# Performance work log

Hardware: AMD Instinct MI355X
Metric: run time of the kernel (lower is better)

The kernel has to match this reference:

```python
import jax, jax.numpy as jnp
import numpy as np

B, N, D, L = 16, 100, 1024, 2000


def setup_inputs() -> dict:
    key = jax.random.key(0)
    ks = jax.random.split(key, 9)
    s = 1.0 / np.sqrt(D)
    return {
        "feature": jax.random.normal(ks[0], (B, N, D), dtype=jnp.float32),
        "graph": jax.random.randint(ks[1], (B, N, N), 0, L),
        "W0": jax.random.normal(ks[2], (D, D), dtype=jnp.float32) * s,
        "W1": jax.random.normal(ks[3], (D, D), dtype=jnp.float32) * s,
        "bias": jax.random.uniform(ks[4], (L, D), dtype=jnp.float32, minval=-s, maxval=s),
        "dp_Wa": jax.random.normal(ks[5], (D, D), dtype=jnp.float32) * s,
        "dp_ba": jax.random.normal(ks[6], (D,), dtype=jnp.float32) * s,
        "dp_Wb": jax.random.normal(ks[7], (D, D), dtype=jnp.float32) * s,
        "dp_bb": jax.random.normal(ks[8], (D,), dtype=jnp.float32) * s,
        "get_alpha": 0,
    }


def reference(feature, graph, W0, W1, bias, dp_Wa, dp_ba, dp_Wb, dp_bb, get_alpha):
    # ---- DirectedGraphConv.conv ----
    adj = (graph != 0).astype(feature.dtype)                     # [B,N,N]
    out = feature + feature @ W0.T + feature @ W1.T              # [B,N,D]
    out = out + jnp.take(bias, graph, axis=0).sum(axis=2)        # label-embedding gather+sum over neighbors
    # ---- relation_alpha: DotProduct(feature, feature) ----
    a = feature @ dp_Wa.T + dp_ba                                # [B,N,D]
    b = feature @ dp_Wb.T + dp_bb                                # [B,N,D]
    alpha = jnp.einsum('bik,bjk->bij', a, b)                     # [B,N,N]
    alpha = jnp.maximum(alpha, 0.0)                              # alpha[alpha<0]=0
    alpha = jnp.einsum('bij,bjk->bik', adj, alpha)               # bmm(adj, alpha)
    alpha = jax.nn.softmax(alpha, axis=1)                        # Softmax(dim=1)
    out = jnp.einsum('bij,bjk->bik', alpha, out)                 # bmm(alpha, output)
    if get_alpha:
        return (out, alpha)
    return out
```

## Files before the change

kernel.cpp:

```cpp
#include <hip/hip_runtime.h>
#include <stdint.h>

#define B_   16
#define N_   100
#define D_   1024
#define L_   2000
#define M_   1600

#define ZCAP 64
#define RCAP 24
#define TC   12

typedef __bf16 bf16x8 __attribute__((ext_vector_type(8)));
typedef float  f32x4  __attribute__((ext_vector_type(4)));

__device__ __forceinline__ void gl_lds16(const __bf16* g, __bf16* l) {
    __builtin_amdgcn_global_load_lds(
        (const __attribute__((address_space(1))) void*)g,
        (__attribute__((address_space(3))) void*)l, 16, 0, 0);
}


__global__ void __launch_bounds__(256)
k_prep(const float* __restrict__ f,
       const float* __restrict__ W0, const float* __restrict__ W1,
       const float* __restrict__ Wa, const float* __restrict__ Wb,
       const float* __restrict__ bias,
       __bf16* __restrict__ fb, __bf16* __restrict__ wcat, __bf16* __restrict__ biasB) {
    int i = blockIdx.x * 256 + threadIdx.x;
    union { __bf16 h[8]; uint4 u; } pk;
    if (i < 204800) {
        long base = (long)i * 8;
        const float4* p = (const float4*)(f + base);
        float4 x = p[0], y = p[1];
        pk.h[0]=(__bf16)x.x; pk.h[1]=(__bf16)x.y; pk.h[2]=(__bf16)x.z; pk.h[3]=(__bf16)x.w;
        pk.h[4]=(__bf16)y.x; pk.h[5]=(__bf16)y.y; pk.h[6]=(__bf16)y.z; pk.h[7]=(__bf16)y.w;
        ((uint4*)fb)[i] = pk.u;
    } else if (i < 598016) {
        int j = i - 204800;
        long base = (long)j * 8;
        long seg = base >> 20;
        long off = base & ((1l << 20) - 1);
        if (seg == 0) {
            const float4* p0 = (const float4*)(W0 + off);
            const float4* p1 = (const float4*)(W1 + off);
            float4 a0 = p0[0], a1 = p0[1], b0 = p1[0], b1 = p1[1];
            pk.h[0]=(__bf16)(a0.x+b0.x); pk.h[1]=(__bf16)(a0.y+b0.y);
            pk.h[2]=(__bf16)(a0.z+b0.z); pk.h[3]=(__bf16)(a0.w+b0.w);
            pk.h[4]=(__bf16)(a1.x+b1.x); pk.h[5]=(__bf16)(a1.y+b1.y);
            pk.h[6]=(__bf16)(a1.z+b1.z); pk.h[7]=(__bf16)(a1.w+b1.w);
        } else {
            const float* src = (seg == 1) ? Wa : Wb;
            const float4* p = (const float4*)(src + off);
            float4 x = p[0], y = p[1];
            pk.h[0]=(__bf16)x.x; pk.h[1]=(__bf16)x.y; pk.h[2]=(__bf16)x.z; pk.h[3]=(__bf16)x.w;
            pk.h[4]=(__bf16)y.x; pk.h[5]=(__bf16)y.y; pk.h[6]=(__bf16)y.z; pk.h[7]=(__bf16)y.w;
        }
        ((uint4*)wcat)[j] = pk.u;
    } else {
        int j = i - 598016;
        long base = (long)j * 8;
        const float4* p = (const float4*)(bias + base);
        float4 x = p[0], y = p[1];
        pk.h[0]=(__bf16)x.x; pk.h[1]=(__bf16)x.y; pk.h[2]=(__bf16)x.z; pk.h[3]=(__bf16)x.w;
        pk.h[4]=(__bf16)y.x; pk.h[5]=(__bf16)y.y; pk.h[6]=(__bf16)y.z; pk.h[7]=(__bf16)y.w;
        ((uint4*)biasB)[j] = pk.u;
    }
}


#define BM 64
#define BN 128
#define BK 64

__global__ void __launch_bounds__(256)
k_gemm(const __bf16* __restrict__ A, const __bf16* __restrict__ Bw,
       const float* __restrict__ feat, const float* __restrict__ ba,
       const float* __restrict__ bbias,
       float* __restrict__ out0, float* __restrict__ aB, float* __restrict__ bB) {
    __shared__ __align__(16) __bf16 As[BM * BK];
    __shared__ __align__(16) __bf16 Bs[BN * BK];
    int t = threadIdx.x;
    int bm = blockIdx.x, bn = blockIdx.y;
    int lane = t & 63, wave = t >> 6;
    int wr = wave & 1, wc = wave >> 1;
    int lrow = lane & 15, quad = lane >> 4;

    f32x4 acc[2][4] = {};
    const __bf16* Ag = A  + (long)(bm * BM) * D_;
    const __bf16* Bg = Bw + (long)(bn * BN) * D_;

    for (int k0 = 0; k0 < D_; k0 += BK) {
        #pragma unroll
        for (int pi = 0; pi < 2; ++pi) {
            int p = pi * 256 + t, row = p >> 3, c = (p & 7) ^ (row & 7);
            gl_lds16(Ag + (long)row * D_ + k0 + c * 8, As + p * 8);
        }
        #pragma unroll
        for (int pi = 0; pi < 4; ++pi) {
            int p = pi * 256 + t, row = p >> 3, c = (p & 7) ^ (row & 7);
            gl_lds16(Bg + (long)row * D_ + k0 + c * 8, Bs + p * 8);
        }
        __syncthreads();
        #pragma unroll
        for (int ks = 0; ks < 2; ++ks) {
            bf16x8 af[2], bf[4];
            #pragma unroll
            for (int i = 0; i < 2; ++i) {
                int r = wr * 32 + i * 16 + lrow;
                int slot = r * 8 + (((ks << 2) | quad) ^ (r & 7));
                af[i] = *(const bf16x8*)(As + slot * 8);
            }
            #pragma unroll
            for (int j = 0; j < 4; ++j) {
                int r = wc * 64 + j * 16 + lrow;
                int slot = r * 8 + (((ks << 2) | quad) ^ (r & 7));
                bf[j] = *(const bf16x8*)(Bs + slot * 8);
            }
            #pragma unroll
            for (int i = 0; i < 2; ++i)
                #pragma unroll
                for (int j = 0; j < 4; ++j)
                    acc[i][j] = __builtin_amdgcn_mfma_f32_16x16x32_bf16(af[i], bf[j], acc[i][j], 0, 0, 0);
        }
        __syncthreads();
    }

    int nbase = bn * BN;
    int seg = nbase >> 10;
    #pragma unroll
    for (int i = 0; i < 2; ++i) {
        int gm0 = bm * BM + wr * 32 + i * 16 + quad * 4;
        #pragma unroll
        for (int j = 0; j < 4; ++j) {
            int col = (nbase + wc * 64 + j * 16 + lrow) & 1023;
            #pragma unroll
            for (int r = 0; r < 4; ++r) {
                long m = gm0 + r;
                float v = acc[i][j][r];
                if (seg == 0)      out0[m * D_ + col] = v + feat[m * D_ + col];
                else if (seg == 1) aB[m * D_ + col]   = v + ba[col];
                else               bB[m * D_ + col]   = v + bbias[col];
            }
        }
    }
}


__global__ void __launch_bounds__(256)
k_gather(const int* __restrict__ graph, const __bf16* __restrict__ biasB,
         float* __restrict__ out0) {
    int bi = blockIdx.x;
    int t = threadIdx.x;
    __shared__ int idxs[N_];
    if (t < N_) idxs[t] = graph[(long)bi * N_ + t];
    __syncthreads();
    float a0 = 0.f, a1 = 0.f, a2 = 0.f, a3 = 0.f;
    for (int j = 0; j < N_; ++j) {
        int lb = idxs[j];
        union { uint2 u; __bf16 h[4]; } pk;
        pk.u = ((const uint2*)(biasB + (long)lb * D_))[t];
        a0 += (float)pk.h[0]; a1 += (float)pk.h[1];
        a2 += (float)pk.h[2]; a3 += (float)pk.h[3];
    }
    float4* o = (float4*)(out0 + (long)bi * D_) + t;
    float4 cur = *o;
    cur.x += a0; cur.y += a1; cur.z += a2; cur.w += a3;
    *o = cur;
}


__global__ void __launch_bounds__(256)
k_scan(const int* __restrict__ graph, int* __restrict__ meta) {
    int b = blockIdx.x, t = threadIdx.x;
    __shared__ int cnt, ndvS;
    __shared__ int zi[ZCAP], zj[ZCAP], pr[ZCAP], di[RCAP];
    if (t == 0) cnt = 0;
    __syncthreads();
    const int* g = graph + (long)b * N_ * N_;
    for (int p = t; p < N_ * N_; p += 256) {
        if (g[p] == 0) {
            int pos = atomicAdd(&cnt, 1);
            if (pos < ZCAP) { zi[pos] = p / N_; zj[pos] = p % N_; }
        }
    }
    __syncthreads();
    if (t == 0) {
        int Z = min(cnt, ZCAP), n = 0;
        for (int q = 0; q < Z; ++q) {
            int r = -1;
            for (int s = 0; s < n; ++s) if (di[s] == zi[q]) { r = s; break; }
            if (r < 0 && n < RCAP) { di[n] = zi[q]; r = n; ++n; }
            pr[q] = r;
        }
        ndvS = n;
    }
    __syncthreads();
    int Z = min(cnt, ZCAP), n = ndvS;
    int* mb = meta + b * 256;
    if (t == 0) { mb[0] = Z; mb[1] = n; }
    if (t < Z) { mb[2 + t] = zj[t]; mb[66 + t] = pr[t]; }
    if (t < n) mb[130 + t] = di[t];
    if (t < N_) {
        int m = 0;
        for (int r = 0; r < n; ++r) if (di[r] == t) m = 1 + r;
        mb[154 + t] = m;
    }
}


__global__ void __launch_bounds__(256)
k_alpha(const int* __restrict__ meta, const float* __restrict__ aB,
        const float* __restrict__ bB, float* __restrict__ wl, float* __restrict__ cwG) {
    int b = blockIdx.x, kc = blockIdx.y;
    int t = threadIdx.x, lane = t & 63, wave = t >> 6;
    const int* mb = meta + b * 256;
    int Z = mb[0], ndv = mb[1];
    __shared__ int zjL[ZCAP], prL[ZCAP];
    __shared__ float corrL[RCAP][4];
    __shared__ float wred[4][4];
    if (t < Z) { zjL[t] = mb[2 + t]; prL[t] = mb[66 + t]; }
    if (t < RCAP * 4) corrL[t >> 2][t & 3] = 0.f;
    __syncthreads();

    int k0 = kc * 4;
    float4 bv[4];
    #pragma unroll
    for (int kk = 0; kk < 4; ++kk)
        bv[kk] = *(const float4*)(bB + ((long)(b * N_ + k0 + kk)) * D_ + t * 4);

    for (int q = 0; q < Z; ++q) {
        const float* ar = aB + ((long)(b * N_ + zjL[q])) * D_;
        float4 av = *(const float4*)(ar + t * 4);
        float s[4];
        #pragma unroll
        for (int kk = 0; kk < 4; ++kk)
            s[kk] = av.x * bv[kk].x + av.y * bv[kk].y + av.z * bv[kk].z + av.w * bv[kk].w;
        #pragma unroll
        for (int off = 32; off > 0; off >>= 1)
            #pragma unroll
            for (int kk = 0; kk < 4; ++kk) s[kk] += __shfl_xor(s[kk], off);
        if (lane == 0) { wred[wave][0]=s[0]; wred[wave][1]=s[1]; wred[wave][2]=s[2]; wred[wave][3]=s[3]; }
        __syncthreads();
        if (t < 4) {
            float v = wred[0][t] + wred[1][t] + wred[2][t] + wred[3][t];
            v = fmaxf(v, 0.f);
            int r = prL[q];
            if (r >= 0) corrL[r][t] += v;
        }
        __syncthreads();
    }

    if (t < 4) {
        int k = k0 + t;
        float denom = (float)(N_ - ndv);
        for (int r = 0; r < ndv; ++r) {
            float e = __expf(-corrL[r][t]);
            corrL[r][t] = e;
            denom += e;
        }
        float w = 1.f / denom;
        wl[b * N_ + k] = w;
        for (int r = 0; r < ndv; ++r)
            cwG[((long)b * RCAP + r) * N_ + k] = corrL[r][t] * w;
    }
}


__global__ void __launch_bounds__(256)
k_mix(const int* __restrict__ meta, const float* __restrict__ wl,
      const float* __restrict__ cwG, const float* __restrict__ out0,
      float* __restrict__ out) {
    int b = blockIdx.x, dq = blockIdx.y;
    int t = threadIdx.x, c = t & 127, h = t >> 7;
    int d0 = dq * 128;
    const int* mb = meta + b * 256;
    int ndv = mb[1], ntask = ndv + 1;
    __shared__ float wT[TC][N_];
    __shared__ float parts[2][TC][128];
    __shared__ int mapL[N_];
    if (t < N_) mapL[t] = mb[154 + t];

    const float* o0 = out0 + (long)b * N_ * D_ + d0;
    for (int cb = 0; cb < ntask; cb += TC) {
        for (int idx = t; idx < TC * N_; idx += 256) {
            int rr = idx / N_, j = idx - rr * N_;
            int task = cb + rr;
            float v = 0.f;
            if (task == 0)         v = wl[b * N_ + j];
            else if (task <= ndv)  v = cwG[((long)b * RCAP + task - 1) * N_ + j];
            wT[rr][j] = v;
        }
        __syncthreads();
        float acc[TC] = {};
        #pragma unroll 2
        for (int j = h * 50; j < h * 50 + 50; ++j) {
            float v = o0[(long)j * D_ + c];
            #pragma unroll
            for (int rr = 0; rr < TC; ++rr) acc[rr] += wT[rr][j] * v;
        }
        #pragma unroll
        for (int rr = 0; rr < TC; ++rr) parts[h][rr][c] = acc[rr];
        __syncthreads();
        for (int i = h * 50; i < h * 50 + 50; ++i) {
            int task = mapL[i];
            if (task >= cb && task < cb + TC) {
                int rr = task - cb;
                out[((long)(b * N_ + i)) * D_ + d0 + c] = parts[0][rr][c] + parts[1][rr][c];
            }
        }
        __syncthreads();
    }
}


extern "C" void kernel_launch(void* const* d_in, const int* in_sizes, int n_in,
                              void* d_out, int out_size, void* d_ws, size_t ws_size,
                              hipStream_t stream) {
    const float* feature = (const float*)d_in[0];
    const int*   graph   = (const int*)d_in[1];
    const float* W0      = (const float*)d_in[2];
    const float* W1      = (const float*)d_in[3];
    const float* bias    = (const float*)d_in[4];
    const float* dp_Wa   = (const float*)d_in[5];
    const float* dp_ba   = (const float*)d_in[6];
    const float* dp_Wb   = (const float*)d_in[7];
    const float* dp_bb   = (const float*)d_in[8];
    float* out = (float*)d_out;

    char* w = (char*)d_ws;
    __bf16* fb16  = (__bf16*)(w);
    __bf16* wcat  = (__bf16*)(w + 3276800);
    __bf16* biasB = (__bf16*)(w + 9568256);
    float*  out0  = (float*)(w + 13664256);
    float*  aB    = (float*)(w + 20217856);
    float*  bB    = (float*)(w + 26771456);
    int*    meta  = (int*)(w + 33325056);
    float*  wl    = (float*)(w + 33341440);
    float*  cwG   = (float*)(w + 33347840);

    k_prep<<<3336, 256, 0, stream>>>(feature, W0, W1, dp_Wa, dp_Wb, bias,
                                     fb16, wcat, biasB);
    k_gemm<<<dim3(25, 24), 256, 0, stream>>>(fb16, wcat, feature, dp_ba, dp_bb,
                                             out0, aB, bB);
    k_gather<<<1600, 256, 0, stream>>>(graph, biasB, out0);
    k_scan<<<B_, 256, 0, stream>>>(graph, meta);
    k_alpha<<<dim3(B_, 25), 256, 0, stream>>>(meta, aB, bB, wl, cwG);
    k_mix<<<dim3(B_, 8), 256, 0, stream>>>(meta, wl, cwG, out0, out);
}
```

Baseline: 179.3 us.

## Fold zero-scan into alpha and mix kernels, halve GEMM N tile

Removes the separate k_scan launch. k_alpha and k_mix now each rebuild the zero-entry metadata from the graph themselves, and k_alpha uses a deterministic per-row layout with a much larger zero capacity. The GEMM N tile drops from 128 to 64, doubling the grid to 1200 blocks for better occupancy across CUs. The gather loop also gets unrolled. In exchange, the graph scan is repeated inside every alpha and mix block (400 + 128 blocks), and each block serialises a 100-element prefix on one thread.

```diff
diff --git a/kernel.cpp b/kernel.cpp
--- a/kernel.cpp
+++ b/kernel.cpp
@@ -7,8 +7,8 @@
 #define L_   2000
 #define M_   1600
 
-#define ZCAP 64
 #define RCAP 24
+#define ZMAX 2400
 #define TC   12
 
 typedef __bf16 bf16x8 __attribute__((ext_vector_type(8)));
@@ -70,7 +70,7 @@
 
 
 #define BM 64
-#define BN 128
+#define BN 64
 #define BK 64
 
 __global__ void __launch_bounds__(256)
@@ -86,7 +86,7 @@
     int wr = wave & 1, wc = wave >> 1;
     int lrow = lane & 15, quad = lane >> 4;
 
-    f32x4 acc[2][4] = {};
+    f32x4 acc[2][2] = {};
     const __bf16* Ag = A  + (long)(bm * BM) * D_;
     const __bf16* Bg = Bw + (long)(bn * BN) * D_;
 
@@ -97,14 +97,14 @@
             gl_lds16(Ag + (long)row * D_ + k0 + c * 8, As + p * 8);
         }
         #pragma unroll
-        for (int pi = 0; pi < 4; ++pi) {
+        for (int pi = 0; pi < 2; ++pi) {
             int p = pi * 256 + t, row = p >> 3, c = (p & 7) ^ (row & 7);
             gl_lds16(Bg + (long)row * D_ + k0 + c * 8, Bs + p * 8);
         }
         __syncthreads();
         #pragma unroll
         for (int ks = 0; ks < 2; ++ks) {
-            bf16x8 af[2], bf[4];
+            bf16x8 af[2], bf[2];
             #pragma unroll
             for (int i = 0; i < 2; ++i) {
                 int r = wr * 32 + i * 16 + lrow;
@@ -112,28 +112,28 @@
                 af[i] = *(const bf16x8*)(As + slot * 8);
             }
             #pragma unroll
-            for (int j = 0; j < 4; ++j) {
-                int r = wc * 64 + j * 16 + lrow;
+            for (int j = 0; j < 2; ++j) {
+                int r = wc * 32 + j * 16 + lrow;
                 int slot = r * 8 + (((ks << 2) | quad) ^ (r & 7));
                 bf[j] = *(const bf16x8*)(Bs + slot * 8);
             }
             #pragma unroll
             for (int i = 0; i < 2; ++i)
                 #pragma unroll
-                for (int j = 0; j < 4; ++j)
+                for (int j = 0; j < 2; ++j)
                     acc[i][j] = __builtin_amdgcn_mfma_f32_16x16x32_bf16(af[i], bf[j], acc[i][j], 0, 0, 0);
         }
         __syncthreads();
     }
 
     int nbase = bn * BN;
-    int seg = nbase >> 10;
+    int seg = bn >> 4;
     #pragma unroll
     for (int i = 0; i < 2; ++i) {
         int gm0 = bm * BM + wr * 32 + i * 16 + quad * 4;
         #pragma unroll
-        for (int j = 0; j < 4; ++j) {
-            int col = (nbase + wc * 64 + j * 16 + lrow) & 1023;
+        for (int j = 0; j < 2; ++j) {
+            int col = (nbase + wc * 32 + j * 16 + lrow) & 1023;
             #pragma unroll
             for (int r = 0; r < 4; ++r) {
                 long m = gm0 + r;
@@ -156,6 +156,7 @@
     if (t < N_) idxs[t] = graph[(long)bi * N_ + t];
     __syncthreads();
     float a0 = 0.f, a1 = 0.f, a2 = 0.f, a3 = 0.f;
+    #pragma unroll 4
     for (int j = 0; j < N_; ++j) {
         int lb = idxs[j];
         union { uint2 u; __bf16 h[4]; } pk;
@@ -171,57 +172,42 @@
 
 
 __global__ void __launch_bounds__(256)
-k_scan(const int* __restrict__ graph, int* __restrict__ meta) {
-    int b = blockIdx.x, t = threadIdx.x;
-    __shared__ int cnt, ndvS;
-    __shared__ int zi[ZCAP], zj[ZCAP], pr[ZCAP], di[RCAP];
-    if (t == 0) cnt = 0;
-    __syncthreads();
-    const int* g = graph + (long)b * N_ * N_;
-    for (int p = t; p < N_ * N_; p += 256) {
-        if (g[p] == 0) {
-            int pos = atomicAdd(&cnt, 1);
-            if (pos < ZCAP) { zi[pos] = p / N_; zj[pos] = p % N_; }
-        }
-    }
-    __syncthreads();
-    if (t == 0) {
-        int Z = min(cnt, ZCAP), n = 0;
-        for (int q = 0; q < Z; ++q) {
-            int r = -1;
-            for (int s = 0; s < n; ++s) if (di[s] == zi[q]) { r = s; break; }
-            if (r < 0 && n < RCAP) { di[n] = zi[q]; r = n; ++n; }
-            pr[q] = r;
-        }
-        ndvS = n;
-    }
-    __syncthreads();
-    int Z = min(cnt, ZCAP), n = ndvS;
-    int* mb = meta + b * 256;
-    if (t == 0) { mb[0] = Z; mb[1] = n; }
-    if (t < Z) { mb[2 + t] = zj[t]; mb[66 + t] = pr[t]; }
-    if (t < n) mb[130 + t] = di[t];
-    if (t < N_) {
-        int m = 0;
-        for (int r = 0; r < n; ++r) if (di[r] == t) m = 1 + r;
-        mb[154 + t] = m;
-    }
-}
-
-
-__global__ void __launch_bounds__(256)
-k_alpha(const int* __restrict__ meta, const float* __restrict__ aB,
+k_alpha(const int* __restrict__ graph, const float* __restrict__ aB,
         const float* __restrict__ bB, float* __restrict__ wl, float* __restrict__ cwG) {
     int b = blockIdx.x, kc = blockIdx.y;
     int t = threadIdx.x, lane = t & 63, wave = t >> 6;
-    const int* mb = meta + b * 256;
-    int Z = mb[0], ndv = mb[1];
-    __shared__ int zjL[ZCAP], prL[ZCAP];
+    __shared__ int rowCnt[N_], rowOff[N_], rowRank[N_];
+    __shared__ int ndvS, totZS;
+    __shared__ int zjL[ZMAX];
+    __shared__ short prL[ZMAX];
     __shared__ float corrL[RCAP][4];
     __shared__ float wred[4][4];
-    if (t < Z) { zjL[t] = mb[2 + t]; prL[t] = mb[66 + t]; }
+
+    const int* g = graph + (long)b * N_ * N_;
+    if (t < N_) {
+        int c = 0;
+        for (int j = 0; j < N_; ++j) if (g[t * N_ + j] == 0) ++c;
+        rowCnt[t] = c;
+    }
     if (t < RCAP * 4) corrL[t >> 2][t & 3] = 0.f;
     __syncthreads();
+    if (t == 0) {
+        int off = 0, rank = 0;
+        for (int i = 0; i < N_; ++i) {
+            if (rowCnt[i] > 0 && rank < RCAP) {
+                rowRank[i] = rank; rowOff[i] = off; off += rowCnt[i]; ++rank;
+            } else rowRank[i] = -1;
+        }
+        ndvS = rank; totZS = off;
+    }
+    __syncthreads();
+    if (t < N_ && rowRank[t] >= 0) {
+        int pos = rowOff[t], r = rowRank[t];
+        for (int j = 0; j < N_; ++j)
+            if (g[t * N_ + j] == 0) { zjL[pos] = j; prL[pos] = (short)r; ++pos; }
+    }
+    __syncthreads();
+    int Z = totZS, ndv = ndvS;
 
     int k0 = kc * 4;
     float4 bv[4];
@@ -244,9 +230,7 @@
         __syncthreads();
         if (t < 4) {
             float v = wred[0][t] + wred[1][t] + wred[2][t] + wred[3][t];
-            v = fmaxf(v, 0.f);
-            int r = prL[q];
-            if (r >= 0) corrL[r][t] += v;
+            corrL[prL[q]][t] += fmaxf(v, 0.f);
         }
         __syncthreads();
     }
@@ -268,18 +252,35 @@
 
 
 __global__ void __launch_bounds__(256)
-k_mix(const int* __restrict__ meta, const float* __restrict__ wl,
+k_mix(const int* __restrict__ graph, const float* __restrict__ wl,
       const float* __restrict__ cwG, const float* __restrict__ out0,
       float* __restrict__ out) {
     int b = blockIdx.x, dq = blockIdx.y;
     int t = threadIdx.x, c = t & 127, h = t >> 7;
     int d0 = dq * 128;
-    const int* mb = meta + b * 256;
-    int ndv = mb[1], ntask = ndv + 1;
+    __shared__ int hasZ[N_], mapL[N_], ndvS;
     __shared__ float wT[TC][N_];
     __shared__ float parts[2][TC][128];
-    __shared__ int mapL[N_];
-    if (t < N_) mapL[t] = mb[154 + t];
+
+    const int* g = graph + (long)b * N_ * N_;
+    if (t < N_) {
+        int z = 0;
+        for (int j = 0; j < N_; ++j) if (g[t * N_ + j] == 0) { z = 1; break; }
+        hasZ[t] = z;
+    }
+    __syncthreads();
+    if (t < N_) {
+        int rank = 0;
+        for (int i = 0; i < t; ++i) rank += hasZ[i];
+        mapL[t] = (hasZ[t] && rank < RCAP) ? 1 + rank : 0;
+    }
+    if (t == 0) {
+        int n = 0;
+        for (int i = 0; i < N_; ++i) n += hasZ[i];
+        ndvS = min(n, RCAP);
+    }
+    __syncthreads();
+    int ndv = ndvS, ntask = ndv + 1;
 
     const float* o0 = out0 + (long)b * N_ * D_ + d0;
     for (int cb = 0; cb < ntask; cb += TC) {
@@ -335,16 +336,14 @@
     float*  out0  = (float*)(w + 13664256);
     float*  aB    = (float*)(w + 20217856);
     float*  bB    = (float*)(w + 26771456);
-    int*    meta  = (int*)(w + 33325056);
-    float*  wl    = (float*)(w + 33341440);
-    float*  cwG   = (float*)(w + 33347840);
+    float*  wl    = (float*)(w + 33325056);
+    float*  cwG   = (float*)(w + 33331456);
 
     k_prep<<<3336, 256, 0, stream>>>(feature, W0, W1, dp_Wa, dp_Wb, bias,
                                      fb16, wcat, biasB);
-    k_gemm<<<dim3(25, 24), 256, 0, stream>>>(fb16, wcat, feature, dp_ba, dp_bb,
+    k_gemm<<<dim3(25, 48), 256, 0, stream>>>(fb16, wcat, feature, dp_ba, dp_bb,
                                              out0, aB, bB);
     k_gather<<<1600, 256, 0, stream>>>(graph, biasB, out0);
-    k_scan<<<B_, 256, 0, stream>>>(graph, meta);
-    k_alpha<<<dim3(B_, 25), 256, 0, stream>>>(meta, aB, bB, wl, cwG);
-    k_mix<<<dim3(B_, 8), 256, 0, stream>>>(meta, wl, cwG, out0, out);
-}
+    k_alpha<<<dim3(B_, 25), 256, 0, stream>>>(graph, aB, bB, wl, cwG);
+    k_mix<<<dim3(B_, 8), 256, 0, stream>>>(graph, wl, cwG, out0, out);
+}
```

Result: slower. 189.0 us (+5.4%).
